# Kernel optimization log

Hardware: AMD Instinct MI355X
Metric: run time of the kernel (lower is better)

## Reference

```python
import math
import jax, jax.numpy as jnp
import numpy as np

B, C, HH, WW = 1, 256, 64, 64
NUM_HEADS = 8
GROUPS = 8
EPS = 1e-5


def setup_inputs() -> dict:
    key = jax.random.key(0)
    ks = jax.random.split(key, 5)
    x = jax.random.normal(ks[0], (B, C, HH, WW), dtype=jnp.float32)
    gn_gamma = jnp.ones((C,), dtype=jnp.float32)
    gn_beta = jnp.zeros((C,), dtype=jnp.float32)
    qkv_w = jax.random.normal(ks[1], (3 * C, C), dtype=jnp.float32) / math.sqrt(C)
    qkv_b = jax.random.normal(ks[2], (3 * C,), dtype=jnp.float32) * 0.02
    proj_w = jax.random.normal(ks[3], (C, C), dtype=jnp.float32) / math.sqrt(C)
    proj_b = jax.random.normal(ks[4], (C,), dtype=jnp.float32) * 0.02
    return {"x": x, "gn_gamma": gn_gamma, "gn_beta": gn_beta,
            "qkv_w": qkv_w, "qkv_b": qkv_b, "proj_w": proj_w, "proj_b": proj_b}


def reference(x, gn_gamma, gn_beta, qkv_w, qkv_b, proj_w, proj_b):
    b, c, h, w = x.shape
    t = h * w
    xf = x.reshape(b, c, t)
    # GroupNorm(8, C): normalize over (C/8 channels x T spatial) per group
    xg = xf.reshape(b, GROUPS, (c // GROUPS) * t)
    mean = xg.mean(axis=-1, keepdims=True)
    var = xg.var(axis=-1, keepdims=True)
    xn = ((xg - mean) * jax.lax.rsqrt(var + EPS)).reshape(b, c, t)
    xn = xn * gn_gamma[:, None] + gn_beta[:, None]
    # 1x1 Conv1d C -> 3C is a channel matmul
    qkv = jnp.einsum('oc,bct->bot', qkv_w, xn) + qkv_b[:, None]  # [b, 3C, t]
    nh = NUM_HEADS
    ch = c // nh
    q, k, v = jnp.split(qkv, 3, axis=1)  # each [b, C, t]
    q = q.reshape(b * nh, ch, t)
    k = k.reshape(b * nh, ch, t)
    v = v.reshape(b * nh, ch, t)
    scale = 1.0 / math.sqrt(math.sqrt(ch))
    weight = jnp.einsum('bct,bcs->bts', q * scale, k * scale)  # [b*nh, t, t]
    weight = jax.nn.softmax(weight.astype(jnp.float32), axis=-1).astype(qkv.dtype)
    a = jnp.einsum('bts,bcs->bct', weight, v).reshape(b, c, t)
    hout = jnp.einsum('oc,bct->bot', proj_w, a) + proj_b[:, None]
    return x + hout.reshape(b, c, h, w)
```

## Files before the change

### kernel.cpp

```cpp
#include <hip/hip_runtime.h>
#include <hip/hip_bf16.h>
#include <math.h>

#define C_DIM 256
#define T_DIM 4096
#define NHEADS 8
#define NGROUPS 8
#define NSPLIT 4
#define SRANGE (T_DIM / NSPLIT)
#define NT (SRANGE / 64)

typedef __attribute__((ext_vector_type(8))) short bf16x8;
typedef __attribute__((ext_vector_type(4))) float f32x4;

#if __has_builtin(__builtin_amdgcn_exp2f)
#define EXP2(x) __builtin_amdgcn_exp2f(x)
#else
#define EXP2(x) exp2f(x)
#endif

#define MFMA16(a, b, c) __builtin_amdgcn_mfma_f32_16x16x32_bf16(a, b, c, 0, 0, 0)

#define WS_PSUM 0
#define WS_PSQ  256
#define WS_MEAN 512
#define WS_RSTD 520
#define WS_QT_F   1024
#define WS_KT_F   (WS_QT_F + 524288)
#define WS_VB_F   (WS_KT_F + 524288)
#define WS_WQB_F  (WS_VB_F + 524288)
#define WS_WPB_F  (WS_WQB_F + 98304)
#define WS_OP_F   (WS_WPB_F + 32768)
#define WS_L_F    (WS_OP_F + NSPLIT * 256 * 4096 / 2)

#define QSCALE 0.2550348527f

__device__ __forceinline__ ushort f2bf(float f) {
  union { float f; unsigned u; } v; v.f = f;
  return (ushort)((v.u + 0x7fffu + ((v.u >> 16) & 1u)) >> 16);
}

__device__ __forceinline__ float bf2f(ushort u) {
  union { unsigned u; float f; } v; v.u = ((unsigned)u) << 16;
  return v.f;
}

__device__ __forceinline__ uint pk2(float a, float b) {
  __hip_bfloat162 h = __float22bfloat162_rn(make_float2(a, b));
  union { __hip_bfloat162 h; uint u; } c; c.h = h; return c.u;
}

__global__ __launch_bounds__(256) void gn_partial(const float* __restrict__ x,
                                                  float* __restrict__ ws) {
  const int g = blockIdx.y;
  const int bx = blockIdx.x;
  const size_t base = (size_t)g * 131072 + (size_t)bx * 4096;
  float s = 0.f, s2 = 0.f;
  for (int i = threadIdx.x; i < 4096; i += 256) {
    float v = x[base + i];
    s += v;
    s2 += v * v;
  }
#pragma unroll
  for (int mask = 1; mask <= 32; mask <<= 1) {
    s += __shfl_xor(s, mask, 64);
    s2 += __shfl_xor(s2, mask, 64);
  }
  __shared__ float red[8];
  const int wid = threadIdx.x >> 6;
  if ((threadIdx.x & 63) == 0) { red[wid] = s; red[4 + wid] = s2; }
  __syncthreads();
  if (threadIdx.x == 0) {
    ws[WS_PSUM + g * 32 + bx] = red[0] + red[1] + red[2] + red[3];
    ws[WS_PSQ + g * 32 + bx] = red[4] + red[5] + red[6] + red[7];
  }
}

__global__ void gn_finalize(float* __restrict__ ws) {
  const int g = blockIdx.x;
  float s = ws[WS_PSUM + g * 32 + threadIdx.x];
  float s2 = ws[WS_PSQ + g * 32 + threadIdx.x];
#pragma unroll
  for (int mask = 1; mask <= 16; mask <<= 1) {
    s += __shfl_xor(s, mask, 32);
    s2 += __shfl_xor(s2, mask, 32);
  }
  if (threadIdx.x == 0) {
    const float inv_n = 1.0f / 131072.0f;
    float mean = s * inv_n;
    float var = s2 * inv_n - mean * mean;
    ws[WS_MEAN + g] = mean;
    ws[WS_RSTD + g] = rsqrtf(var + 1e-5f);
  }
}

__global__ __launch_bounds__(256) void w2bf(const float* __restrict__ wq,
                                            const float* __restrict__ wp,
                                            ushort* __restrict__ wqb,
                                            ushort* __restrict__ wpb) {
  const int i4 = (blockIdx.x * 256 + threadIdx.x) * 4;
  const int n1 = 768 * 256;
  if (i4 < n1) {
    float4 v = *(const float4*)(wq + i4);
    union { ushort us[4]; uint2 u; } pk;
    pk.us[0] = f2bf(v.x); pk.us[1] = f2bf(v.y); pk.us[2] = f2bf(v.z); pk.us[3] = f2bf(v.w);
    *(uint2*)(wqb + i4) = pk.u;
  } else {
    const int j = i4 - n1;
    float4 v = *(const float4*)(wp + j);
    union { ushort us[4]; uint2 u; } pk;
    pk.us[0] = f2bf(v.x); pk.us[1] = f2bf(v.y); pk.us[2] = f2bf(v.z); pk.us[3] = f2bf(v.w);
    *(uint2*)(wpb + j) = pk.u;
  }
}

__global__ __launch_bounds__(256) void qkv_mfma(const float* __restrict__ x,
                                                const float* __restrict__ gamma,
                                                const float* __restrict__ beta,
                                                const float* __restrict__ ws,
                                                const ushort* __restrict__ wqb,
                                                const float* __restrict__ bias,
                                                ushort* __restrict__ qt,
                                                ushort* __restrict__ kt,
                                                ushort* __restrict__ vb) {
  const int t0 = blockIdx.x * 16;
  const int oc = blockIdx.y;
  const int obase = oc * 256;
  __shared__ ushort A[16 * 256];
  __shared__ float fg[256], fb[256];
  const int tid = threadIdx.x;
  {
    const int c = tid, gg = c >> 5;
    float rstd = ws[WS_RSTD + gg], mean = ws[WS_MEAN + gg];
    float fgv = gamma[c] * rstd;
    fg[c] = fgv; fb[c] = beta[c] - mean * fgv;
  }
  __syncthreads();
#pragma unroll
  for (int pass = 0; pass < 4; ++pass) {
    const int c = pass * 64 + (tid >> 2);
    const int tin = (tid & 3) * 4;
    float4 xv = *(const float4*)(x + (size_t)c * T_DIM + t0 + tin);
    const float fgc = fg[c], fbc = fb[c];
    float xn[4] = {fmaf(xv.x, fgc, fbc), fmaf(xv.y, fgc, fbc),
                   fmaf(xv.z, fgc, fbc), fmaf(xv.w, fgc, fbc)};
#pragma unroll
    for (int i = 0; i < 4; ++i) {
      const int t = tin + i;
      A[t * 256 + (c ^ ((t & 7) << 3))] = f2bf(xn[i]);
    }
  }
  __syncthreads();

  const int w = tid >> 6, lane = tid & 63, l15 = lane & 15, g = lane >> 4;
  const int o0 = obase + w * 64;
  f32x4 acc[4] = {};
  const ushort* wrow[4];
#pragma unroll
  for (int j = 0; j < 4; ++j)
    wrow[j] = wqb + (size_t)(o0 + 16 * j + l15) * 256;

#pragma unroll
  for (int kk = 0; kk < 8; ++kk) {
    const bf16x8 af = *(const bf16x8*)(&A[l15 * 256 + ((kk * 32 + 8 * g) ^ ((l15 & 7) << 3))]);
#pragma unroll
    for (int j = 0; j < 4; ++j) {
      const bf16x8 bfr = *(const bf16x8*)(wrow[j] + kk * 32 + 8 * g);
      acc[j] = MFMA16(af, bfr, acc[j]);
    }
  }

#pragma unroll
  for (int j = 0; j < 4; ++j) {
    const int o = o0 + 16 * j + l15;
    const float bo = bias[o];
    const int tb = t0 + 4 * g;
    if (oc == 0) {
      const int hh = o >> 5, d = o & 31;
#pragma unroll
      for (int r = 0; r < 4; ++r)
        qt[((size_t)hh * T_DIM + tb + r) * 32 + d] = f2bf((acc[j][r] + bo) * QSCALE);
    } else if (oc == 1) {
      const int oo = o - 256;
      const int hh = oo >> 5, d = oo & 31;
#pragma unroll
      for (int r = 0; r < 4; ++r)
        kt[((size_t)hh * T_DIM + tb + r) * 32 + d] = f2bf(acc[j][r] + bo);
    } else {
      union { ushort us[4]; uint2 u; } pk;
#pragma unroll
      for (int r = 0; r < 4; ++r) pk.us[r] = f2bf(acc[j][r] + bo);
      *(uint2*)(vb + (size_t)(o - 512) * T_DIM + tb) = pk.u;
    }
  }
}

__global__ __launch_bounds__(512, 8) void attn_fwd(const ushort* __restrict__ qt,
                                                   const ushort* __restrict__ kt,
                                                   const ushort* __restrict__ vb,
                                                   ushort* __restrict__ Op,
                                                   float* __restrict__ Lb) {
  const int bid = blockIdx.x;
  const int h = bid & 7;
  const int inner = bid >> 3;
  const int qb = inner & 31;
  const int z = inner >> 5;
  const int tid = threadIdx.x;
  const int w = tid >> 6, lane = tid & 63, l15 = lane & 15, g = lane >> 4;

  __shared__ ushort Klds[2][64 * 40];
  __shared__ ushort Vlds[2][32 * 72];
  __shared__ ushort Plds[8][16 * 72];

  const int t_a = qb * 128 + w * 16 + l15;
  const bf16x8 qf = *(const bf16x8*)(qt + ((size_t)(h * T_DIM + t_a) * 32 + 8 * g));

  f32x4 O0 = {}, O1 = {};
  float la = 0.f;

  const int sbeg = z * SRANGE;
  const ushort* kgp = kt + (size_t)h * T_DIM * 32 + (size_t)(sbeg + (tid >> 3)) * 32 + (tid & 7) * 4;
  const ushort* vgp = vb + (size_t)(h * 32 + (tid >> 4)) * T_DIM + sbeg + (tid & 15) * 4;
  ushort* kw0 = &Klds[0][(tid >> 3) * 40 + (tid & 7) * 4];
  ushort* vw0 = &Vlds[0][(tid >> 4) * 72 + (tid & 15) * 4];

  {
    uint2 k0 = *(const uint2*)kgp;
    uint2 v0 = *(const uint2*)vgp;
    *(uint2*)kw0 = k0;
    *(uint2*)vw0 = v0;
  }
  __syncthreads();

  ushort* prow = &Plds[w][l15 * 72];
  int cur = 0;
  for (int t = 0; t < NT; ++t) {
    uint2 kn, vn;
    const bool more = (t + 1 < NT);
    if (more) {
      kn = *(const uint2*)(kgp + (size_t)(t + 1) * 2048);
      vn = *(const uint2*)(vgp + (t + 1) * 64);
    }

    const ushort* kbase = &Klds[cur][0];
    const f32x4 z4 = {};
    const bf16x8 kf0 = *(const bf16x8*)(kbase + (0 * 16 + l15) * 40 + 8 * g);
    const bf16x8 kf1 = *(const bf16x8*)(kbase + (1 * 16 + l15) * 40 + 8 * g);
    __builtin_amdgcn_s_setprio(1);
    f32x4 s0 = MFMA16(kf0, qf, z4);
    f32x4 s1 = MFMA16(kf1, qf, z4);
    __builtin_amdgcn_s_setprio(0);
    const bf16x8 kf2 = *(const bf16x8*)(kbase + (2 * 16 + l15) * 40 + 8 * g);
    const bf16x8 kf3 = *(const bf16x8*)(kbase + (3 * 16 + l15) * 40 + 8 * g);
    __builtin_amdgcn_s_setprio(1);
    f32x4 s2 = MFMA16(kf2, qf, z4);
    f32x4 s3 = MFMA16(kf3, qf, z4);
    __builtin_amdgcn_s_setprio(0);

    float rsum;
    {
      float p0, p1, p2, p3;
      uint2 pv;
      p0 = EXP2(s0[0]); p1 = EXP2(s0[1]); p2 = EXP2(s0[2]); p3 = EXP2(s0[3]);
      rsum = (p0 + p1) + (p2 + p3);
      pv.x = pk2(p0, p1); pv.y = pk2(p2, p3);
      *(uint2*)(prow + 0 * 16 + 4 * g) = pv;
      p0 = EXP2(s1[0]); p1 = EXP2(s1[1]); p2 = EXP2(s1[2]); p3 = EXP2(s1[3]);
      rsum += (p0 + p1) + (p2 + p3);
      pv.x = pk2(p0, p1); pv.y = pk2(p2, p3);
      *(uint2*)(prow + 1 * 16 + 4 * g) = pv;
      p0 = EXP2(s2[0]); p1 = EXP2(s2[1]); p2 = EXP2(s2[2]); p3 = EXP2(s2[3]);
      rsum += (p0 + p1) + (p2 + p3);
      pv.x = pk2(p0, p1); pv.y = pk2(p2, p3);
      *(uint2*)(prow + 2 * 16 + 4 * g) = pv;
      p0 = EXP2(s3[0]); p1 = EXP2(s3[1]); p2 = EXP2(s3[2]); p3 = EXP2(s3[3]);
      rsum += (p0 + p1) + (p2 + p3);
      pv.x = pk2(p0, p1); pv.y = pk2(p2, p3);
      *(uint2*)(prow + 3 * 16 + 4 * g) = pv;
    }
    la += rsum;

    const ushort* vbase = &Vlds[cur][0];
    const bf16x8 pf0 = *(const bf16x8*)(prow + 8 * g);
    const bf16x8 pf1 = *(const bf16x8*)(prow + 32 + 8 * g);
    const bf16x8 vf00 = *(const bf16x8*)(vbase + (l15) * 72 + 8 * g);
    const bf16x8 vf01 = *(const bf16x8*)(vbase + (l15) * 72 + 32 + 8 * g);
    const bf16x8 vf10 = *(const bf16x8*)(vbase + (16 + l15) * 72 + 8 * g);
    const bf16x8 vf11 = *(const bf16x8*)(vbase + (16 + l15) * 72 + 32 + 8 * g);
    __builtin_amdgcn_s_setprio(1);
    O0 = MFMA16(vf00, pf0, O0);
    O0 = MFMA16(vf01, pf1, O0);
    O1 = MFMA16(vf10, pf0, O1);
    O1 = MFMA16(vf11, pf1, O1);
    __builtin_amdgcn_s_setprio(0);

    if (more) {
      *(uint2*)(kw0 + (cur ^ 1) * (64 * 40)) = kn;
      *(uint2*)(vw0 + (cur ^ 1) * (32 * 72)) = vn;
    }
    __syncthreads();
    cur ^= 1;
  }

  ushort* opz = Op + (size_t)(z * NHEADS + h) * 32 * T_DIM;
#pragma unroll
  for (int r = 0; r < 4; ++r) {
    const int d0 = 4 * g + r;
    opz[(size_t)d0 * T_DIM + t_a]        = f2bf(O0[r]);
    opz[(size_t)(16 + d0) * T_DIM + t_a] = f2bf(O1[r]);
  }
  la += __shfl_xor(la, 16, 64);
  la += __shfl_xor(la, 32, 64);
  if (g == 0)
    Lb[(size_t)(z * NHEADS + h) * T_DIM + t_a] = la;
}

__global__ __launch_bounds__(256) void proj_mfma(const ushort* __restrict__ Op,
                                                 const float* __restrict__ Lb,
                                                 const ushort* __restrict__ wpb,
                                                 const float* __restrict__ bias,
                                                 const float* __restrict__ x,
                                                 float* __restrict__ out) {
  const int t0 = blockIdx.x * 16;
  __shared__ ushort A[16 * 256];
  __shared__ float rinv[128];
  const int tid = threadIdx.x;
  if (tid < 128) {
    const int h = tid >> 4, tt = tid & 15;
    float l = 0.f;
#pragma unroll
    for (int zz = 0; zz < NSPLIT; ++zz)
      l += Lb[(size_t)(zz * NHEADS + h) * T_DIM + t0 + tt];
    rinv[tid] = 1.0f / l;
  }
  __syncthreads();
#pragma unroll
  for (int pass = 0; pass < 4; ++pass) {
    const int c = pass * 64 + (tid >> 2);
    const int h = c >> 5;
    const int tin = (tid & 3) * 4;
    float a4[4] = {0.f, 0.f, 0.f, 0.f};
#pragma unroll
    for (int zz = 0; zz < NSPLIT; ++zz) {
      uint2 v = *(const uint2*)(Op + (size_t)(zz * 256 + c) * T_DIM + t0 + tin);
      const ushort* us = (const ushort*)&v;
#pragma unroll
      for (int i = 0; i < 4; ++i) a4[i] += bf2f(us[i]);
    }
#pragma unroll
    for (int i = 0; i < 4; ++i) {
      const int t = tin + i;
      A[t * 256 + (c ^ ((t & 7) << 3))] = f2bf(a4[i] * rinv[(h << 4) | t]);
    }
  }
  __syncthreads();

  const int w = tid >> 6, lane = tid & 63, l15 = lane & 15, g = lane >> 4;
  const int o0 = blockIdx.y * 128 + w * 32;
  f32x4 acc[2] = {};
  const ushort* wrow[2];
#pragma unroll
  for (int j = 0; j < 2; ++j)
    wrow[j] = wpb + (size_t)(o0 + 16 * j + l15) * 256;

#pragma unroll
  for (int kk = 0; kk < 8; ++kk) {
    const bf16x8 af = *(const bf16x8*)(&A[l15 * 256 + ((kk * 32 + 8 * g) ^ ((l15 & 7) << 3))]);
#pragma unroll
    for (int j = 0; j < 2; ++j) {
      const bf16x8 bfr = *(const bf16x8*)(wrow[j] + kk * 32 + 8 * g);
      acc[j] = MFMA16(af, bfr, acc[j]);
    }
  }

#pragma unroll
  for (int j = 0; j < 2; ++j) {
    const int o = o0 + 16 * j + l15;
    const float bo = bias[o];
    const size_t base = (size_t)o * T_DIM + t0 + 4 * g;
    const float4 xr = *(const float4*)(x + base);
    float4 ov;
    ov.x = acc[j][0] + bo + xr.x;
    ov.y = acc[j][1] + bo + xr.y;
    ov.z = acc[j][2] + bo + xr.z;
    ov.w = acc[j][3] + bo + xr.w;
    *(float4*)(out + base) = ov;
  }
}

extern "C" void kernel_launch(void* const* d_in, const int* in_sizes, int n_in,
                              void* d_out, int out_size, void* d_ws, size_t ws_size,
                              hipStream_t stream) {
  const float* x      = (const float*)d_in[0];
  const float* gamma  = (const float*)d_in[1];
  const float* beta   = (const float*)d_in[2];
  const float* qkv_w  = (const float*)d_in[3];
  const float* qkv_b  = (const float*)d_in[4];
  const float* proj_w = (const float*)d_in[5];
  const float* proj_b = (const float*)d_in[6];
  float* out = (float*)d_out;
  float* ws  = (float*)d_ws;

  ushort* qt  = (ushort*)(ws + WS_QT_F);
  ushort* kt  = (ushort*)(ws + WS_KT_F);
  ushort* vb  = (ushort*)(ws + WS_VB_F);
  ushort* wqb = (ushort*)(ws + WS_WQB_F);
  ushort* wpb = (ushort*)(ws + WS_WPB_F);
  ushort* Op  = (ushort*)(ws + WS_OP_F);
  float*  Lb  = ws + WS_L_F;

  gn_partial<<<dim3(32, NGROUPS), 256, 0, stream>>>(x, ws);
  gn_finalize<<<NGROUPS, 32, 0, stream>>>(ws);
  w2bf<<<256, 256, 0, stream>>>(qkv_w, proj_w, wqb, wpb);
  qkv_mfma<<<dim3(256, 3), 256, 0, stream>>>(x, gamma, beta, ws, wqb, qkv_b, qt, kt, vb);
  attn_fwd<<<NHEADS * 32 * NSPLIT, 512, 0, stream>>>(qt, kt, vb, Op, Lb);
  proj_mfma<<<dim3(256, 2), 256, 0, stream>>>(Op, Lb, wpb, proj_b, x, out);
}
```

Baseline: 77.40 us.

## Process two query tiles per attention block, merge qkv blocks and fold GN finalize

The attention kernel now handles 256 queries per block (two 16-row query fragments per wave) and reuses each K/V LDS tile for both, which halves the grid and the K/V global and LDS traffic per query. The qkv projection is merged into one 512-thread block per 16-token tile that computes all 768 outputs with software-prefetched weight fragments, so the normalized input tile is built once instead of three times. The GroupNorm finalize step moves into the weight conversion kernel, removing one launch. In exchange, register pressure and LDS use per attention block go up and fewer blocks are available to fill the GPU.

```diff
diff --git a/kernel.cpp b/kernel.cpp
--- a/kernel.cpp
+++ b/kernel.cpp
@@ -76,28 +76,11 @@
   }
 }
 
-__global__ void gn_finalize(float* __restrict__ ws) {
-  const int g = blockIdx.x;
-  float s = ws[WS_PSUM + g * 32 + threadIdx.x];
-  float s2 = ws[WS_PSQ + g * 32 + threadIdx.x];
-#pragma unroll
-  for (int mask = 1; mask <= 16; mask <<= 1) {
-    s += __shfl_xor(s, mask, 32);
-    s2 += __shfl_xor(s2, mask, 32);
-  }
-  if (threadIdx.x == 0) {
-    const float inv_n = 1.0f / 131072.0f;
-    float mean = s * inv_n;
-    float var = s2 * inv_n - mean * mean;
-    ws[WS_MEAN + g] = mean;
-    ws[WS_RSTD + g] = rsqrtf(var + 1e-5f);
-  }
-}
-
-__global__ __launch_bounds__(256) void w2bf(const float* __restrict__ wq,
-                                            const float* __restrict__ wp,
-                                            ushort* __restrict__ wqb,
-                                            ushort* __restrict__ wpb) {
+__global__ __launch_bounds__(256) void w2bf_gn(const float* __restrict__ wq,
+                                               const float* __restrict__ wp,
+                                               float* __restrict__ ws,
+                                               ushort* __restrict__ wqb,
+                                               ushort* __restrict__ wpb) {
   const int i4 = (blockIdx.x * 256 + threadIdx.x) * 4;
   const int n1 = 768 * 256;
   if (i4 < n1) {
@@ -112,9 +95,26 @@
     pk.us[0] = f2bf(v.x); pk.us[1] = f2bf(v.y); pk.us[2] = f2bf(v.z); pk.us[3] = f2bf(v.w);
     *(uint2*)(wpb + j) = pk.u;
   }
-}
-
-__global__ __launch_bounds__(256) void qkv_mfma(const float* __restrict__ x,
+  if (blockIdx.x == 0) {
+    const int g = threadIdx.x >> 5, idx = threadIdx.x & 31;
+    float s = ws[WS_PSUM + g * 32 + idx];
+    float s2 = ws[WS_PSQ + g * 32 + idx];
+#pragma unroll
+    for (int mask = 1; mask <= 16; mask <<= 1) {
+      s += __shfl_xor(s, mask, 32);
+      s2 += __shfl_xor(s2, mask, 32);
+    }
+    if (idx == 0) {
+      const float inv_n = 1.0f / 131072.0f;
+      float mean = s * inv_n;
+      float var = s2 * inv_n - mean * mean;
+      ws[WS_MEAN + g] = mean;
+      ws[WS_RSTD + g] = rsqrtf(var + 1e-5f);
+    }
+  }
+}
+
+__global__ __launch_bounds__(512) void qkv_mfma(const float* __restrict__ x,
                                                 const float* __restrict__ gamma,
                                                 const float* __restrict__ beta,
                                                 const float* __restrict__ ws,
@@ -124,12 +124,10 @@
                                                 ushort* __restrict__ kt,
                                                 ushort* __restrict__ vb) {
   const int t0 = blockIdx.x * 16;
-  const int oc = blockIdx.y;
-  const int obase = oc * 256;
   __shared__ ushort A[16 * 256];
   __shared__ float fg[256], fb[256];
   const int tid = threadIdx.x;
-  {
+  if (tid < 256) {
     const int c = tid, gg = c >> 5;
     float rstd = ws[WS_RSTD + gg], mean = ws[WS_MEAN + gg];
     float fgv = gamma[c] * rstd;
@@ -137,9 +135,10 @@
   }
   __syncthreads();
 #pragma unroll
-  for (int pass = 0; pass < 4; ++pass) {
-    const int c = pass * 64 + (tid >> 2);
-    const int tin = (tid & 3) * 4;
+  for (int p = 0; p < 2; ++p) {
+    const int idx = p * 512 + tid;
+    const int c = idx >> 2;
+    const int tin = (idx & 3) * 4;
     float4 xv = *(const float4*)(x + (size_t)c * T_DIM + t0 + tin);
     const float fgc = fg[c], fbc = fb[c];
     float xn[4] = {fmaf(xv.x, fgc, fbc), fmaf(xv.y, fgc, fbc),
@@ -153,34 +152,42 @@
   __syncthreads();
 
   const int w = tid >> 6, lane = tid & 63, l15 = lane & 15, g = lane >> 4;
-  const int o0 = obase + w * 64;
-  f32x4 acc[4] = {};
-  const ushort* wrow[4];
-#pragma unroll
-  for (int j = 0; j < 4; ++j)
-    wrow[j] = wqb + (size_t)(o0 + 16 * j + l15) * 256;
+  const int ob = w * 96;
+  f32x4 acc[6] = {};
+  const ushort* wrow[6];
+#pragma unroll
+  for (int j = 0; j < 6; ++j)
+    wrow[j] = wqb + (size_t)(ob + j * 16 + l15) * 256;
+
+  bf16x8 bc[6], bn[6];
+#pragma unroll
+  for (int j = 0; j < 6; ++j) bc[j] = *(const bf16x8*)(wrow[j] + 8 * g);
 
 #pragma unroll
   for (int kk = 0; kk < 8; ++kk) {
     const bf16x8 af = *(const bf16x8*)(&A[l15 * 256 + ((kk * 32 + 8 * g) ^ ((l15 & 7) << 3))]);
-#pragma unroll
-    for (int j = 0; j < 4; ++j) {
-      const bf16x8 bfr = *(const bf16x8*)(wrow[j] + kk * 32 + 8 * g);
-      acc[j] = MFMA16(af, bfr, acc[j]);
-    }
-  }
-
-#pragma unroll
-  for (int j = 0; j < 4; ++j) {
-    const int o = o0 + 16 * j + l15;
+    if (kk < 7) {
+#pragma unroll
+      for (int j = 0; j < 6; ++j) bn[j] = *(const bf16x8*)(wrow[j] + (kk + 1) * 32 + 8 * g);
+    }
+#pragma unroll
+    for (int j = 0; j < 6; ++j)
+      acc[j] = MFMA16(af, bc[j], acc[j]);
+#pragma unroll
+    for (int j = 0; j < 6; ++j) bc[j] = bn[j];
+  }
+
+#pragma unroll
+  for (int j = 0; j < 6; ++j) {
+    const int o = ob + j * 16 + l15;
     const float bo = bias[o];
     const int tb = t0 + 4 * g;
-    if (oc == 0) {
+    if (o < 256) {
       const int hh = o >> 5, d = o & 31;
 #pragma unroll
       for (int r = 0; r < 4; ++r)
         qt[((size_t)hh * T_DIM + tb + r) * 32 + d] = f2bf((acc[j][r] + bo) * QSCALE);
-    } else if (oc == 1) {
+    } else if (o < 512) {
       const int oo = o - 256;
       const int hh = oo >> 5, d = oo & 31;
 #pragma unroll
@@ -195,7 +202,7 @@
   }
 }
 
-__global__ __launch_bounds__(512, 8) void attn_fwd(const ushort* __restrict__ qt,
+__global__ __launch_bounds__(512, 4) void attn_fwd(const ushort* __restrict__ qt,
                                                    const ushort* __restrict__ kt,
                                                    const ushort* __restrict__ vb,
                                                    ushort* __restrict__ Op,
@@ -203,36 +210,36 @@
   const int bid = blockIdx.x;
   const int h = bid & 7;
   const int inner = bid >> 3;
-  const int qb = inner & 31;
-  const int z = inner >> 5;
+  const int qb = inner & 15;
+  const int z = inner >> 4;
   const int tid = threadIdx.x;
   const int w = tid >> 6, lane = tid & 63, l15 = lane & 15, g = lane >> 4;
 
   __shared__ ushort Klds[2][64 * 40];
   __shared__ ushort Vlds[2][32 * 72];
-  __shared__ ushort Plds[8][16 * 72];
-
-  const int t_a = qb * 128 + w * 16 + l15;
-  const bf16x8 qf = *(const bf16x8*)(qt + ((size_t)(h * T_DIM + t_a) * 32 + 8 * g));
-
-  f32x4 O0 = {}, O1 = {};
-  float la = 0.f;
+  __shared__ ushort Plds[8][16 * 144];
+
+  const int t_a = qb * 256 + w * 16 + l15;
+  const int t_b = t_a + 128;
+  const bf16x8 qfa = *(const bf16x8*)(qt + ((size_t)(h * T_DIM + t_a) * 32 + 8 * g));
+  const bf16x8 qfb = *(const bf16x8*)(qt + ((size_t)(h * T_DIM + t_b) * 32 + 8 * g));
+
+  f32x4 Oa0 = {}, Oa1 = {}, Ob0 = {}, Ob1 = {};
+  float la = 0.f, lb = 0.f;
 
   const int sbeg = z * SRANGE;
   const ushort* kgp = kt + (size_t)h * T_DIM * 32 + (size_t)(sbeg + (tid >> 3)) * 32 + (tid & 7) * 4;
   const ushort* vgp = vb + (size_t)(h * 32 + (tid >> 4)) * T_DIM + sbeg + (tid & 15) * 4;
   ushort* kw0 = &Klds[0][(tid >> 3) * 40 + (tid & 7) * 4];
   ushort* vw0 = &Vlds[0][(tid >> 4) * 72 + (tid & 15) * 4];
-
   {
-    uint2 k0 = *(const uint2*)kgp;
-    uint2 v0 = *(const uint2*)vgp;
-    *(uint2*)kw0 = k0;
-    *(uint2*)vw0 = v0;
-  }
-  __syncthreads();
-
-  ushort* prow = &Plds[w][l15 * 72];
+    *(uint2*)kw0 = *(const uint2*)kgp;
+    *(uint2*)vw0 = *(const uint2*)vgp;
+  }
+  __syncthreads();
+
+  ushort* prow_a = &Plds[w][l15 * 144];
+  ushort* prow_b = prow_a + 72;
   int cur = 0;
   for (int t = 0; t < NT; ++t) {
     uint2 kn, vn;
@@ -243,55 +250,86 @@
     }
 
     const ushort* kbase = &Klds[cur][0];
+    const ushort* vbase = &Vlds[cur][0];
     const f32x4 z4 = {};
     const bf16x8 kf0 = *(const bf16x8*)(kbase + (0 * 16 + l15) * 40 + 8 * g);
     const bf16x8 kf1 = *(const bf16x8*)(kbase + (1 * 16 + l15) * 40 + 8 * g);
-    __builtin_amdgcn_s_setprio(1);
-    f32x4 s0 = MFMA16(kf0, qf, z4);
-    f32x4 s1 = MFMA16(kf1, qf, z4);
-    __builtin_amdgcn_s_setprio(0);
     const bf16x8 kf2 = *(const bf16x8*)(kbase + (2 * 16 + l15) * 40 + 8 * g);
     const bf16x8 kf3 = *(const bf16x8*)(kbase + (3 * 16 + l15) * 40 + 8 * g);
     __builtin_amdgcn_s_setprio(1);
-    f32x4 s2 = MFMA16(kf2, qf, z4);
-    f32x4 s3 = MFMA16(kf3, qf, z4);
+    f32x4 sa0 = MFMA16(kf0, qfa, z4);
+    f32x4 sa1 = MFMA16(kf1, qfa, z4);
+    f32x4 sa2 = MFMA16(kf2, qfa, z4);
+    f32x4 sa3 = MFMA16(kf3, qfa, z4);
+    f32x4 sb0 = MFMA16(kf0, qfb, z4);
+    f32x4 sb1 = MFMA16(kf1, qfb, z4);
+    f32x4 sb2 = MFMA16(kf2, qfb, z4);
+    f32x4 sb3 = MFMA16(kf3, qfb, z4);
     __builtin_amdgcn_s_setprio(0);
 
-    float rsum;
     {
-      float p0, p1, p2, p3;
-      uint2 pv;
-      p0 = EXP2(s0[0]); p1 = EXP2(s0[1]); p2 = EXP2(s0[2]); p3 = EXP2(s0[3]);
+      float p0, p1, p2, p3; uint2 pv; float rsum;
+      p0 = EXP2(sa0[0]); p1 = EXP2(sa0[1]); p2 = EXP2(sa0[2]); p3 = EXP2(sa0[3]);
       rsum = (p0 + p1) + (p2 + p3);
       pv.x = pk2(p0, p1); pv.y = pk2(p2, p3);
-      *(uint2*)(prow + 0 * 16 + 4 * g) = pv;
-      p0 = EXP2(s1[0]); p1 = EXP2(s1[1]); p2 = EXP2(s1[2]); p3 = EXP2(s1[3]);
-      rsum += (p0 + p1) + (p2 + p3);
-      pv.x = pk2(p0, p1); pv.y = pk2(p2, p3);
-      *(uint2*)(prow + 1 * 16 + 4 * g) = pv;
-      p0 = EXP2(s2[0]); p1 = EXP2(s2[1]); p2 = EXP2(s2[2]); p3 = EXP2(s2[3]);
-      rsum += (p0 + p1) + (p2 + p3);
-      pv.x = pk2(p0, p1); pv.y = pk2(p2, p3);
-      *(uint2*)(prow + 2 * 16 + 4 * g) = pv;
-      p0 = EXP2(s3[0]); p1 = EXP2(s3[1]); p2 = EXP2(s3[2]); p3 = EXP2(s3[3]);
-      rsum += (p0 + p1) + (p2 + p3);
-      pv.x = pk2(p0, p1); pv.y = pk2(p2, p3);
-      *(uint2*)(prow + 3 * 16 + 4 * g) = pv;
-    }
-    la += rsum;
-
-    const ushort* vbase = &Vlds[cur][0];
-    const bf16x8 pf0 = *(const bf16x8*)(prow + 8 * g);
-    const bf16x8 pf1 = *(const bf16x8*)(prow + 32 + 8 * g);
+      *(uint2*)(prow_a + 0 * 16 + 4 * g) = pv;
+      p0 = EXP2(sa1[0]); p1 = EXP2(sa1[1]); p2 = EXP2(sa1[2]); p3 = EXP2(sa1[3]);
+      rsum += (p0 + p1) + (p2 + p3);
+      pv.x = pk2(p0, p1); pv.y = pk2(p2, p3);
+      *(uint2*)(prow_a + 1 * 16 + 4 * g) = pv;
+      p0 = EXP2(sa2[0]); p1 = EXP2(sa2[1]); p2 = EXP2(sa2[2]); p3 = EXP2(sa2[3]);
+      rsum += (p0 + p1) + (p2 + p3);
+      pv.x = pk2(p0, p1); pv.y = pk2(p2, p3);
+      *(uint2*)(prow_a + 2 * 16 + 4 * g) = pv;
+      p0 = EXP2(sa3[0]); p1 = EXP2(sa3[1]); p2 = EXP2(sa3[2]); p3 = EXP2(sa3[3]);
+      rsum += (p0 + p1) + (p2 + p3);
+      pv.x = pk2(p0, p1); pv.y = pk2(p2, p3);
+      *(uint2*)(prow_a + 3 * 16 + 4 * g) = pv;
+      la += rsum;
+    }
+
     const bf16x8 vf00 = *(const bf16x8*)(vbase + (l15) * 72 + 8 * g);
     const bf16x8 vf01 = *(const bf16x8*)(vbase + (l15) * 72 + 32 + 8 * g);
     const bf16x8 vf10 = *(const bf16x8*)(vbase + (16 + l15) * 72 + 8 * g);
     const bf16x8 vf11 = *(const bf16x8*)(vbase + (16 + l15) * 72 + 32 + 8 * g);
+
+    const bf16x8 pfa0 = *(const bf16x8*)(prow_a + 8 * g);
+    const bf16x8 pfa1 = *(const bf16x8*)(prow_a + 32 + 8 * g);
     __builtin_amdgcn_s_setprio(1);
-    O0 = MFMA16(vf00, pf0, O0);
-    O0 = MFMA16(vf01, pf1, O0);
-    O1 = MFMA16(vf10, pf0, O1);
-    O1 = MFMA16(vf11, pf1, O1);
+    Oa0 = MFMA16(vf00, pfa0, Oa0);
+    Oa0 = MFMA16(vf01, pfa1, Oa0);
+    Oa1 = MFMA16(vf10, pfa0, Oa1);
+    Oa1 = MFMA16(vf11, pfa1, Oa1);
+    __builtin_amdgcn_s_setprio(0);
+
+    {
+      float p0, p1, p2, p3; uint2 pv; float rsum;
+      p0 = EXP2(sb0[0]); p1 = EXP2(sb0[1]); p2 = EXP2(sb0[2]); p3 = EXP2(sb0[3]);
+      rsum = (p0 + p1) + (p2 + p3);
+      pv.x = pk2(p0, p1); pv.y = pk2(p2, p3);
+      *(uint2*)(prow_b + 0 * 16 + 4 * g) = pv;
+      p0 = EXP2(sb1[0]); p1 = EXP2(sb1[1]); p2 = EXP2(sb1[2]); p3 = EXP2(sb1[3]);
+      rsum += (p0 + p1) + (p2 + p3);
+      pv.x = pk2(p0, p1); pv.y = pk2(p2, p3);
+      *(uint2*)(prow_b + 1 * 16 + 4 * g) = pv;
+      p0 = EXP2(sb2[0]); p1 = EXP2(sb2[1]); p2 = EXP2(sb2[2]); p3 = EXP2(sb2[3]);
+      rsum += (p0 + p1) + (p2 + p3);
+      pv.x = pk2(p0, p1); pv.y = pk2(p2, p3);
+      *(uint2*)(prow_b + 2 * 16 + 4 * g) = pv;
+      p0 = EXP2(sb3[0]); p1 = EXP2(sb3[1]); p2 = EXP2(sb3[2]); p3 = EXP2(sb3[3]);
+      rsum += (p0 + p1) + (p2 + p3);
+      pv.x = pk2(p0, p1); pv.y = pk2(p2, p3);
+      *(uint2*)(prow_b + 3 * 16 + 4 * g) = pv;
+      lb += rsum;
+    }
+
+    const bf16x8 pfb0 = *(const bf16x8*)(prow_b + 8 * g);
+    const bf16x8 pfb1 = *(const bf16x8*)(prow_b + 32 + 8 * g);
+    __builtin_amdgcn_s_setprio(1);
+    Ob0 = MFMA16(vf00, pfb0, Ob0);
+    Ob0 = MFMA16(vf01, pfb1, Ob0);
+    Ob1 = MFMA16(vf10, pfb0, Ob1);
+    Ob1 = MFMA16(vf11, pfb1, Ob1);
     __builtin_amdgcn_s_setprio(0);
 
     if (more) {
@@ -306,13 +344,19 @@
 #pragma unroll
   for (int r = 0; r < 4; ++r) {
     const int d0 = 4 * g + r;
-    opz[(size_t)d0 * T_DIM + t_a]        = f2bf(O0[r]);
-    opz[(size_t)(16 + d0) * T_DIM + t_a] = f2bf(O1[r]);
+    opz[(size_t)d0 * T_DIM + t_a]        = f2bf(Oa0[r]);
+    opz[(size_t)(16 + d0) * T_DIM + t_a] = f2bf(Oa1[r]);
+    opz[(size_t)d0 * T_DIM + t_b]        = f2bf(Ob0[r]);
+    opz[(size_t)(16 + d0) * T_DIM + t_b] = f2bf(Ob1[r]);
   }
   la += __shfl_xor(la, 16, 64);
   la += __shfl_xor(la, 32, 64);
-  if (g == 0)
+  lb += __shfl_xor(lb, 16, 64);
+  lb += __shfl_xor(lb, 32, 64);
+  if (g == 0) {
     Lb[(size_t)(z * NHEADS + h) * T_DIM + t_a] = la;
+    Lb[(size_t)(z * NHEADS + h) * T_DIM + t_b] = lb;
+  }
 }
 
 __global__ __launch_bounds__(256) void proj_mfma(const ushort* __restrict__ Op,
@@ -410,9 +454,8 @@
   float*  Lb  = ws + WS_L_F;
 
   gn_partial<<<dim3(32, NGROUPS), 256, 0, stream>>>(x, ws);
-  gn_finalize<<<NGROUPS, 32, 0, stream>>>(ws);
-  w2bf<<<256, 256, 0, stream>>>(qkv_w, proj_w, wqb, wpb);
-  qkv_mfma<<<dim3(256, 3), 256, 0, stream>>>(x, gamma, beta, ws, wqb, qkv_b, qt, kt, vb);
-  attn_fwd<<<NHEADS * 32 * NSPLIT, 512, 0, stream>>>(qt, kt, vb, Op, Lb);
+  w2bf_gn<<<256, 256, 0, stream>>>(qkv_w, proj_w, ws, wqb, wpb);
+  qkv_mfma<<<256, 512, 0, stream>>>(x, gamma, beta, ws, wqb, qkv_b, qt, kt, vb);
+  attn_fwd<<<NHEADS * 16 * NSPLIT, 512, 0, stream>>>(qt, kt, vb, Op, Lb);
   proj_mfma<<<dim3(256, 2), 256, 0, stream>>>(Op, Lb, wpb, proj_b, x, out);
 }
```

New measurement: 73.63 us. 4.9% less time.
